# Kernel optimization log

Hardware: AMD Instinct MI355X
Metric: run time of the kernel (lower is better)

The kernel has to match this reference:

```python
import jax, jax.numpy as jnp
import numpy as np

VARIANCE = 1.0  # prototorch euclidean_similarity default


def setup_inputs() -> dict:
    key = jax.random.key(0)
    k1, k2, k3 = jax.random.split(key, 3)
    B, D = 32768, 1024
    K, C = 5, 3  # sum([2,1,2]) components, len([2,1,2]) classes
    x = jax.random.normal(k1, (B, D), dtype=jnp.float32)
    components = jax.random.normal(k2, (K, D), dtype=jnp.float32)
    # PPRI: random probabilistic reasonings in [0,1], shape [K, C, 2]
    reasonings = jax.random.uniform(k3, (K, C, 2), dtype=jnp.float32)
    return {"x": x, "components": components, "reasonings": reasonings}


def reference(x, components, reasonings):
    # --- euclidean similarity: exp(-d(x, c)^2 / (2*variance)) ---
    # squared pairwise distances via expansion (avoids [B,K,D] intermediate)
    x2 = jnp.sum(x * x, axis=-1, keepdims=True)          # [B,1]
    c2 = jnp.sum(components * components, axis=-1)       # [K]
    d2 = x2 + c2[None, :] - 2.0 * (x @ components.T)     # [B,K]
    d2 = jnp.maximum(d2, 0.0)
    sims = jnp.exp(-d2 / (2.0 * VARIANCE))               # [B,K]

    # --- cbcc competition ---
    # reasonings [K,C,2] -> permute(2,1,0) -> [2,C,K], clamp to [0,1]
    R = jnp.clip(jnp.transpose(reasonings, (2, 1, 0)), 0.0, 1.0)
    A, Bneg = R[0], R[1]                                 # each [C,K]
    pk = A
    nk = (1.0 - A) * Bneg                                # [C,K]
    numerator = sims @ (pk - nk).T + jnp.sum(nk, axis=1) # [B,C]
    probs = numerator / jnp.sum(pk + nk, axis=1)         # [B,C]
    return probs
```

## Files before the change

kernel.cpp:

```cpp
#include <hip/hip_runtime.h>


#define DD 1024
#define KK 5
#define CC 3
#define F4R (DD / 4)
#define JN (F4R / 64)

__global__ __launch_bounds__(256, 4) void cbc_kernel(
    const float* __restrict__ x,
    const float* __restrict__ comps,
    const float* __restrict__ reas,
    float* __restrict__ out,
    int B)
{
    __shared__ float4 cl[KK * F4R];

    const int tid  = threadIdx.x;
    const int lane = tid & 63;
    const int waves_per_block = blockDim.x >> 6;
    const int wave    = blockIdx.x * waves_per_block + (tid >> 6);
    const int n_waves = gridDim.x * waves_per_block;

    const float4* c4 = (const float4*)comps;
    for (int i = tid; i < KK * F4R; i += blockDim.x) cl[i] = c4[i];

    const int c = (lane < CC) ? lane : 0;
    float wv[KK], bias = 0.f, den = 0.f;
#pragma unroll
    for (int k = 0; k < KK; ++k) {
        float a = reas[k * (CC * 2) + c * 2 + 0];
        float b = reas[k * (CC * 2) + c * 2 + 1];
        a = fminf(fmaxf(a, 0.f), 1.f);
        b = fminf(fmaxf(b, 0.f), 1.f);
        float nk = (1.f - a) * b;
        wv[k] = a - nk;
        bias += nk;
        den  += a + nk;
    }
    const float invden = 1.f / den;

    __syncthreads();

    const float4* x4 = (const float4*)x;

    for (int row = wave; row < B; row += n_waves) {
        const float4* p = x4 + (size_t)row * F4R + lane;

        float acc[KK];
#pragma unroll
        for (int k = 0; k < KK; ++k) acc[k] = 0.f;

#pragma unroll
        for (int j = 0; j < JN; ++j) {
            float4 xv = p[j * 64];
#pragma unroll
            for (int k = 0; k < KK; ++k) {
                float4 cv = cl[k * F4R + j * 64 + lane];
                float dx = xv.x - cv.x;
                float dy = xv.y - cv.y;
                float dz = xv.z - cv.z;
                float dw = xv.w - cv.w;
                acc[k] += dx * dx;
                acc[k] += dy * dy;
                acc[k] += dz * dz;
                acc[k] += dw * dw;
            }
        }

#pragma unroll
        for (int k = 0; k < KK; ++k) {
#pragma unroll
            for (int off = 32; off > 0; off >>= 1)
                acc[k] += __shfl_xor(acc[k], off, 64);
        }

        if (lane < CC) {
            float num = bias;
#pragma unroll
            for (int k = 0; k < KK; ++k)
                num += __expf(-0.5f * acc[k]) * wv[k];
            out[(size_t)row * CC + lane] = num * invden;
        }
    }
}

extern "C" void kernel_launch(void* const* d_in, const int* in_sizes, int n_in,
                              void* d_out, int out_size, void* d_ws, size_t ws_size,
                              hipStream_t stream) {
    const float* x = (const float*)d_in[0];
    const float* comps = (const float*)d_in[1];
    const float* reas = (const float*)d_in[2];
    float* out = (float*)d_out;
    const int B = in_sizes[0] / DD;

    const int blocks = 2048;
    cbc_kernel<<<blocks, 256, 0, stream>>>(x, comps, reas, out, B);
}
```

Measured before the change: 193.2 us.

## Map each row to eight threads instead of one wavefront

Replaces the wave-per-row grid-stride loop with a fixed mapping where eight threads share one row and each thread walks a contiguous 32-float4 slice. The index is rotated per thread to spread LDS bank accesses. This cuts the cross-lane reduction from six shuffle rounds over 64 lanes to three over 8 lanes, and launches one block per 32 rows. In exchange, global loads in a wavefront are no longer contiguous across lanes, so they rely on caching to stay coalesced.

```diff
diff --git a/kernel.cpp b/kernel.cpp
--- a/kernel.cpp
+++ b/kernel.cpp
@@ -1,11 +1,13 @@
 #include <hip/hip_runtime.h>
 
 
-#define DD 1024
-#define KK 5
-#define CC 3
+#define DD  1024
+#define KK  5
+#define CC  3
+#define QS  8
+#define RPB 32
 #define F4R (DD / 4)
-#define JN (F4R / 64)
+#define F4T (F4R / QS)
 
 __global__ __launch_bounds__(256, 4) void cbc_kernel(
     const float* __restrict__ x,
@@ -16,16 +18,15 @@
 {
     __shared__ float4 cl[KK * F4R];
 
-    const int tid  = threadIdx.x;
-    const int lane = tid & 63;
-    const int waves_per_block = blockDim.x >> 6;
-    const int wave    = blockIdx.x * waves_per_block + (tid >> 6);
-    const int n_waves = gridDim.x * waves_per_block;
+    const int tid = threadIdx.x;
+    const int q   = tid & (QS - 1);
+    const int r   = tid >> 3;
+    const int row = blockIdx.x * RPB + r;
 
     const float4* c4 = (const float4*)comps;
     for (int i = tid; i < KK * F4R; i += blockDim.x) cl[i] = c4[i];
 
-    const int c = (lane < CC) ? lane : 0;
+    const int c = (q < CC) ? q : 0;
     float wv[KK], bias = 0.f, den = 0.f;
 #pragma unroll
     for (int k = 0; k < KK; ++k) {
@@ -42,21 +43,21 @@
 
     __syncthreads();
 
-    const float4* x4 = (const float4*)x;
-
-    for (int row = wave; row < B; row += n_waves) {
-        const float4* p = x4 + (size_t)row * F4R + lane;
+    if (row < B) {
+        const float4* xp = (const float4*)x + (size_t)row * F4R + q * F4T;
+        const int     cb = q * F4T;
 
         float acc[KK];
 #pragma unroll
         for (int k = 0; k < KK; ++k) acc[k] = 0.f;
 
-#pragma unroll
-        for (int j = 0; j < JN; ++j) {
-            float4 xv = p[j * 64];
+#pragma unroll 8
+        for (int i = 0; i < F4T; ++i) {
+            const int ri = (i + q) & (F4T - 1);
+            float4 xv = xp[ri];
 #pragma unroll
             for (int k = 0; k < KK; ++k) {
-                float4 cv = cl[k * F4R + j * 64 + lane];
+                float4 cv = cl[k * F4R + cb + ri];
                 float dx = xv.x - cv.x;
                 float dy = xv.y - cv.y;
                 float dz = xv.z - cv.z;
@@ -70,17 +71,17 @@
 
 #pragma unroll
         for (int k = 0; k < KK; ++k) {
-#pragma unroll
-            for (int off = 32; off > 0; off >>= 1)
-                acc[k] += __shfl_xor(acc[k], off, 64);
+            acc[k] += __shfl_xor(acc[k], 1, 64);
+            acc[k] += __shfl_xor(acc[k], 2, 64);
+            acc[k] += __shfl_xor(acc[k], 4, 64);
         }
 
-        if (lane < CC) {
+        if (q < CC) {
             float num = bias;
 #pragma unroll
             for (int k = 0; k < KK; ++k)
                 num += __expf(-0.5f * acc[k]) * wv[k];
-            out[(size_t)row * CC + lane] = num * invden;
+            out[(size_t)row * CC + q] = num * invden;
         }
     }
 }
@@ -94,6 +95,6 @@
     float* out = (float*)d_out;
     const int B = in_sizes[0] / DD;
 
-    const int blocks = 2048;
+    const int blocks = (B + RPB - 1) / RPB;
     cbc_kernel<<<blocks, 256, 0, stream>>>(x, comps, reas, out, B);
 }
```

Result: slower. 264.4 us (+36.8%).
